# Performance work log

Measured on AMD Instinct MI355X. Metric: run time of the kernel, lower is better.

## Reference

```python
import jax, jax.numpy as jnp
import numpy as np

ALPHA = 0.9
T = 809          # doc_len_limit hard-coded in fofe_tricontext_encoder
M = 16           # opt['max_len'] (cand_len_limit)
BN_EPS = 1e-5


def _cand_indices(T, M):
    # Enumeration order matches get_sample_index: outer over start s, inner over span.
    s_list, e_list = [], []
    for s in range(T):
        for span in range(min(M, T - s)):
            s_list.append(s)
            e_list.append(s + span)
    return np.asarray(s_list, np.int32), np.asarray(e_list, np.int32)

_S_IDX, _E_IDX = _cand_indices(T, M)          # [N_CANDS] = [12824]
_SPAN = (_E_IDX - _S_IDX).astype(np.int64)
# FOFE decay coefficient alpha^(e-s+1) for subtracting the prefix before the span
_COEF = (ALPHA ** (_SPAN + 1)).astype(np.float32)
# Lower-triangular FOFE prefix operator: A[t,k] = alpha^(t-k) for k<=t
_DIFF = np.subtract.outer(np.arange(T), np.arange(T))
_AFWD = np.where(_DIFF >= 0, ALPHA ** np.maximum(_DIFF, 0), 0.0).astype(np.float32)


def _bn(x, g, b, m, v):
    return (x - m) * jax.lax.rsqrt(v + BN_EPS) * g + b


def _forward(doc_emb, query_emb, W1, g1, b1, m1, v1, W2, g2, b2, m2, v2, W3):
    B, Tt, Dd = doc_emb.shape
    A = jnp.asarray(_AFWD)
    # forward FOFE prefixes F[t] = sum_{k<=t} alpha^(t-k) x[k]; inverse FOFE suffixes
    F = jnp.einsum('tk,bkd->btd', A, doc_emb)          # [B,T,Dd]
    R = jnp.einsum('tk,bkd->btd', A.T, doc_emb)        # [B,T,Dd]
    Fp = jnp.concatenate([jnp.zeros((B, 1, Dd), F.dtype), F], axis=1)   # Fp[:,s]=F[s-1]
    Rp = jnp.concatenate([R, jnp.zeros((B, 1, Dd), R.dtype)], axis=1)   # Rp[:,e+1]
    s_idx = jnp.asarray(_S_IDX)
    e_idx = jnp.asarray(_E_IDX)
    coef = jnp.asarray(_COEF)
    lctx = Fp[:, s_idx]                                 # left context excl cand
    cand = F[:, e_idx] - coef[None, :, None] * Fp[:, s_idx]  # FOFE of span [s,e]
    rctx = Rp[:, e_idx + 1]                             # right context excl cand
    doc_fofe = jnp.concatenate([lctx, cand, rctx], axis=-1)  # [B,N,3*Dd]
    # query FOFE (fofe_linear): z = sum_t alpha^(Lq-1-t) q[t]
    Lq = query_emb.shape[1]
    w = (ALPHA ** jnp.arange(Lq - 1, -1, -1, dtype=jnp.float32))
    qf = jnp.einsum('t,btd->bd', w, query_emb)          # [B,E]
    N = doc_fofe.shape[1]
    qf_b = jnp.broadcast_to(qf[:, None, :], (B, N, qf.shape[-1]))
    dq = jnp.concatenate([doc_fofe, qf_b], axis=-1)     # [B,N,3*Dd+E]
    x = dq.reshape(B * N, -1)
    h = jax.nn.relu(_bn(x @ W1.T, g1, b1, m1, v1))      # 1x1 conv == GEMM
    h = jax.nn.relu(_bn(h @ W2.T, g2, b2, m2, v2))
    out = (h @ W3.T).reshape(B, N, 2)                   # 2 class scores per candidate
    return out


def setup_inputs() -> dict:
    key = jax.random.key(0)
    ks = jax.random.split(key, 13)
    B, Lq, Dd, E = 4, 30, 304, 300
    Cin, H4, H2 = 3 * Dd + E, 1024, 512
    return {
        'doc_emb': jax.random.normal(ks[0], (B, T, Dd), jnp.float32),
        'query_emb': jax.random.normal(ks[1], (B, Lq, E), jnp.float32),
        'W1': jax.random.normal(ks[2], (H4, Cin), jnp.float32) / np.sqrt(Cin),
        'g1': jax.random.normal(ks[3], (H4,), jnp.float32),
        'b1': jax.random.normal(ks[4], (H4,), jnp.float32),
        'm1': jax.random.normal(ks[5], (H4,), jnp.float32),
        'v1': jax.random.uniform(ks[6], (H4,), jnp.float32),
        'W2': jax.random.normal(ks[7], (H2, H4), jnp.float32) / np.sqrt(H4),
        'g2': jax.random.normal(ks[8], (H2,), jnp.float32),
        'b2': jax.random.normal(ks[9], (H2,), jnp.float32),
        'm2': jax.random.normal(ks[10], (H2,), jnp.float32),
        'v2': jax.random.uniform(ks[11], (H2,), jnp.float32),
        'W3': jax.random.normal(ks[12], (2, H2), jnp.float32) / np.sqrt(H2),
    }


def reference(doc_emb, query_emb, W1, g1, b1, m1, v1, W2, g2, b2, m2, v2, W3):
    return _forward(doc_emb, query_emb, W1, g1, b1, m1, v1, W2, g2, b2, m2, v2, W3)
```

## Files before the change

### kernel.cpp

```cpp
#include <hip/hip_runtime.h>
#include <hip/hip_fp16.h>
#include <string.h>

#define T_LEN   809
#define DD      304
#define EE      300
#define LQ      30
#define NCAND   12824
#define NPAD    12928
#define CIN     1212
#define H1      1024
#define H2      512
#define BATCH   4
#define MROWS_F (BATCH * NPAD)
#define KS      320
#define TPAD    3328
#define NROWS_U 3240

#define MP_W1      208
#define MP_W2      4048
#define MP_BIAS2   6096
#define MP_BASE    6098
#define MP_RMAP    7122
#define MP_TOTAL   7324

__device__ __constant__ float c_coef[16] = {
  0.9f, 0.81f, 0.729f, 0.6561f, 0.59049f, 0.531441f, 0.4782969f, 0.43046721f,
  0.387420489f, 0.3486784401f, 0.31381059609f, 0.282429536481f,
  0.2541865828329f, 0.22876792454961f, 0.205891132094649f, 0.1853020188851841f
};

__device__ __forceinline__ unsigned short f2h(float f) {
  const __half h = __float2half(f);
  return __half_as_ushort(h);
}
__device__ __forceinline__ unsigned int hadd2u(unsigned int a, unsigned int b) {
  const __half2 r = __hadd2(*reinterpret_cast<const __half2*>(&a),
                            *reinterpret_cast<const __half2*>(&b));
  return *reinterpret_cast<const unsigned int*>(&r);
}
__device__ __forceinline__ unsigned int comb2h(unsigned int ul, unsigned int uc,
                                               unsigned int ue, __half2 ncf2) {
  const __half2 t = __hfma2(*reinterpret_cast<const __half2*>(&uc), ncf2,
                            *reinterpret_cast<const __half2*>(&ue));
  const __half2 r = __hadd2(*reinterpret_cast<const __half2*>(&ul), t);
  unsigned int ru = *reinterpret_cast<const unsigned int*>(&r);
  ru &= ~(((ru >> 15) & 0x10001u) * 0xFFFFu);
  return ru;
}

typedef const __attribute__((address_space(1))) unsigned int GU32;
typedef __attribute__((address_space(3))) unsigned int LU32;
__device__ __forceinline__ void async16(const unsigned short* g, unsigned short* l) {
  __builtin_amdgcn_global_load_lds((GU32*)g, (LU32*)l, 16, 0, 0);
}

__global__ __launch_bounds__(256) void k_prep(const float* __restrict__ doc,
                                              const float* __restrict__ qe,
                                              const float* __restrict__ W1,
                                              const float* __restrict__ g1,
                                              const float* __restrict__ b1,
                                              const float* __restrict__ m1,
                                              const float* __restrict__ v1,
                                              const float* __restrict__ W2,
                                              const float* __restrict__ g2,
                                              const float* __restrict__ b2,
                                              const float* __restrict__ m2,
                                              const float* __restrict__ v2,
                                              unsigned short* __restrict__ Fz,
                                              unsigned short* __restrict__ Rz,
                                              unsigned short* __restrict__ Wlc,
                                              unsigned short* __restrict__ Wr,
                                              unsigned short* __restrict__ W2b,
                                              float* __restrict__ bias2,
                                              float* __restrict__ baseW,
                                              unsigned int* __restrict__ rowmap)
{
  __shared__ float qs[EE];
  const int vb  = blockIdx.x;
  const int tid = threadIdx.x;

  if (vb < MP_W1) {
    const int dchunk = vb & 1;
    const int rest   = vb >> 1;
    const int tchunk = rest % 13;
    const int b      = (rest / 13) & 3;
    const int dir    = rest / 52;
    const int d  = dchunk * 256 + tid;
    const int t0 = tchunk * 64;
    if (dir == 0) {
      if (tchunk == 0 && d < KS) Fz[((size_t)b * 810) * KS + d] = 0;
      if (d >= DD) return;
      const float* db = doc + (size_t)b * T_LEN * DD + d;
      int start = t0 - 96; if (start < 0) start = 0;
      int end = t0 + 63; if (end > T_LEN - 1) end = T_LEN - 1;
      float s = 0.f;
      int t = start;
      #pragma unroll 4
      for (; t < t0; ++t) s = fmaf(0.9f, s, db[(size_t)t * DD]);
      #pragma unroll 4
      for (; t <= end; ++t) {
        s = fmaf(0.9f, s, db[(size_t)t * DD]);
        Fz[((size_t)b * 810 + 1 + t) * KS + d] = f2h(s);
      }
    } else {
      if (tchunk == 0 && d < KS) Rz[((size_t)b * 810 + 809) * KS + d] = 0;
      if (d >= DD) return;
      const float* db = doc + (size_t)b * T_LEN * DD + d;
      int t1 = t0 + 63; if (t1 > T_LEN - 1) t1 = T_LEN - 1;
      int start = t1 + 96; if (start > T_LEN - 1) start = T_LEN - 1;
      float s = 0.f;
      int t = start;
      #pragma unroll 4
      for (; t > t1; --t) s = fmaf(0.9f, s, db[(size_t)t * DD]);
      #pragma unroll 4
      for (; t >= t0; --t) {
        s = fmaf(0.9f, s, db[(size_t)t * DD]);
        Rz[((size_t)b * 810 + t) * KS + d] = f2h(s);
      }
    }
  } else if (vb < MP_W2) {
    const int e = (vb - MP_W1) * 256 + tid;
    const int j = e / KS;
    const int k = e - j * KS;
    int jj, koff; unsigned short* dst; size_t idx;
    if (j < 1024)      { jj = j;        koff = k;       dst = Wlc; idx = (size_t)j * KS + k; }
    else if (j < 2048) { jj = j - 1024; koff = 304 + k; dst = Wlc; idx = (size_t)j * KS + k; }
    else               { jj = j - 2048; koff = 608 + k; dst = Wr;  idx = (size_t)(j - 2048) * KS + k; }
    float w = 0.f;
    if (k < 304) w = W1[(size_t)jj * CIN + koff] * g1[jj] * rsqrtf(v1[jj] + 1e-5f);
    dst[idx] = f2h(w);
  } else if (vb < MP_BIAS2) {
    const int e = (vb - MP_W2) * 256 + tid;
    const int j = e >> 10;
    const int k = e & 1023;
    const float w = W2[(size_t)j * H1 + k] * g2[j] * rsqrtf(v2[j] + 1e-5f);
    W2b[(size_t)j * H1 + k] = f2h(w);
  } else if (vb < MP_BASE) {
    const int i = (vb - MP_BIAS2) * 256 + tid;
    if (i < H2) {
      const float s = g2[i] * rsqrtf(v2[i] + 1e-5f);
      bias2[i] = b2[i] - m2[i] * s;
    }
  } else if (vb < MP_RMAP) {
    const int flat = vb - MP_BASE;
    const int b  = flat >> 8;
    const int jg = flat & 255;
    const float* q = qe + (size_t)b * LQ * EE;
    for (int k = tid; k < EE; k += 256) {
      float s = 0.f;
      for (int t = 0; t < LQ; ++t) s = fmaf(s, 0.9f, q[(size_t)t * EE + k]);
      qs[k] = s;
    }
    __syncthreads();
    const int wv   = tid >> 6;
    const int lane = tid & 63;
    const int j = jg * 4 + wv;
    const float* w = W1 + (size_t)j * CIN + 912;
    float acc = 0.f;
    for (int k = lane; k < EE; k += 64) acc = fmaf(qs[k], w[k], acc);
    #pragma unroll
    for (int off = 32; off; off >>= 1) acc += __shfl_down(acc, off);
    if (lane == 0) {
      const float sc = g1[j] * rsqrtf(v1[j] + 1e-5f);
      baseW[(size_t)b * 2048 + j]        = b1[j] - m1[j] * sc + acc * sc;
      baseW[(size_t)b * 2048 + 1024 + j] = 0.f;
    }
  } else {
    const int g = (vb - MP_RMAP) * 256 + tid;
    const int b  = g / NPAD;
    const int rr = g - b * NPAD;
    unsigned int mv = 0;
    if (rr < NCAND) {
      int s, span;
      if (rr < 12704) { s = rr >> 4; span = rr & 15; }
      else {
        const int x = rr - 12704;
        int d = 0;
        while (d < 14 && x >= (15 * (d + 1) - ((d + 1) * d) / 2)) ++d;
        span = x - (15 * d - (d * (d - 1)) / 2);
        s = 794 + d;
      }
      const unsigned int srow = (unsigned int)(b * 810 + s);
      const unsigned int erow = (unsigned int)(b * 810 + s + span + 1);
      mv = srow | (erow << 12) | ((unsigned int)span << 24);
    }
    rowmap[g] = mv;
  }
}

typedef __attribute__((ext_vector_type(8))) short frag8;
typedef __attribute__((ext_vector_type(4))) float f32x4;

#define GEMM_KLOOP(A_, B_, K_)                                                   \
  __shared__ __align__(16) unsigned short As[2 * 128 * 32];                      \
  __shared__ __align__(16) unsigned short Bs[2 * 128 * 32];                      \
  const int tid  = threadIdx.x;                                                  \
  const int lane = tid & 63;                                                     \
  const int wv   = tid >> 6;                                                     \
  const int wm   = wv & 1, wn = wv >> 1;                                         \
  const int lr = lane >> 2;                                                      \
  const int lc = lane & 3;                                                       \
  const int sc = lc ^ ((lr >> 1) & 3);                                           \
  const unsigned short* gA = A_ + ((size_t)bm * 128 + wv * 32 + lr) * K_ + sc * 8; \
  const unsigned short* gB = B_ + ((size_t)bn * 128 + wv * 32 + lr) * K_ + sc * 8; \
  const size_t row16 = (size_t)16 * K_;                                          \
  f32x4 acc[4][4];                                                               \
  _Pragma("unroll")                                                              \
  for (int i = 0; i < 4; ++i)                                                    \
    _Pragma("unroll")                                                            \
    for (int j = 0; j < 4; ++j) acc[i][j] = (f32x4){0.f, 0.f, 0.f, 0.f};         \
  const int arow = lane & 15;                                                    \
  const int pg   = (lane >> 4) ^ ((arow >> 1) & 3);                              \
  const int aoff = (wm * 64 + arow) * 32 + pg * 8;                               \
  const int boff = (wn * 64 + arow) * 32 + pg * 8;                               \
  async16(gA,         &As[wv * 1024]);                                           \
  async16(gA + row16, &As[wv * 1024 + 512]);                                     \
  async16(gB,         &Bs[wv * 1024]);                                           \
  async16(gB + row16, &Bs[wv * 1024 + 512]);                                     \
  asm volatile("s_waitcnt vmcnt(0)" ::: "memory");                               \
  __builtin_amdgcn_sched_barrier(0);                                             \
  for (int kc = 0; kc < K_; kc += 32) {                                          \
    const int cb = (kc >> 5) & 1, nb = cb ^ 1;                                   \
    __builtin_amdgcn_s_barrier();                                                \
    __builtin_amdgcn_sched_barrier(0);                                           \
    if (kc + 32 < K_) {                                                          \
      async16(gA + kc + 32,         &As[nb * 4096 + wv * 1024]);                 \
      async16(gA + kc + 32 + row16, &As[nb * 4096 + wv * 1024 + 512]);           \
      async16(gB + kc + 32,         &Bs[nb * 4096 + wv * 1024]);                 \
      async16(gB + kc + 32 + row16, &Bs[nb * 4096 + wv * 1024 + 512]);           \
    }                                                                            \
    __builtin_amdgcn_sched_barrier(0);                                           \
    frag8 a[4], b[4];                                                            \
    _Pragma("unroll")                                                            \
    for (int i = 0; i < 4; ++i) a[i] = *(const frag8*)&As[cb * 4096 + aoff + i * 512]; \
    _Pragma("unroll")                                                            \
    for (int i = 0; i < 4; ++i) b[i] = *(const frag8*)&Bs[cb * 4096 + boff + i * 512]; \
    __builtin_amdgcn_s_setprio(1);                                               \
    _Pragma("unroll")                                                            \
    for (int i = 0; i < 4; ++i)                                                  \
      _Pragma("unroll")                                                          \
      for (int j = 0; j < 4; ++j)                                                \
        acc[i][j] = __builtin_amdgcn_mfma_f32_16x16x32_f16(a[i], b[j], acc[i][j], 0, 0, 0); \
    __builtin_amdgcn_s_setprio(0);                                               \
    __builtin_amdgcn_sched_barrier(0);                                           \
    if (kc + 32 < K_) { asm volatile("s_waitcnt vmcnt(0)" ::: "memory"); }       \
    __builtin_amdgcn_sched_barrier(0);                                           \
  }

__global__ __launch_bounds__(256, 4) void k_ugemm(const unsigned short* __restrict__ Fz,
                                                  const unsigned short* __restrict__ Wlc,
                                                  const unsigned short* __restrict__ Rz,
                                                  const unsigned short* __restrict__ Wr,
                                                  const float* __restrict__ baseW,
                                                  unsigned short* __restrict__ UF,
                                                  unsigned short* __restrict__ UR)
{
  int bx = blockIdx.x;
  const int isUF = (bx < 416);
  const unsigned short *Ap, *Bp; unsigned short* Cp; int bn, bm, Nout;
  if (isUF) { Ap = Fz; Bp = Wlc; Cp = UF; bn = bx & 15; bm = bx >> 4; Nout = 2048; }
  else { bx -= 416; Ap = Rz; Bp = Wr; Cp = UR; bn = bx & 7; bm = bx >> 3; Nout = 1024; }
  GEMM_KLOOP(Ap, Bp, KS)

  __syncthreads();
  unsigned short* scr = &As[wv * 1152];
  const int grp   = lane >> 4;
  const int ccolb = bn * 128 + wn * 64;
  const int rowl  = lane >> 2;
  const int cg    = (lane & 3) * 16;
  #pragma unroll
  for (int i = 0; i < 4; ++i) {
    #pragma unroll
    for (int j = 0; j < 4; ++j)
      #pragma unroll
      for (int r = 0; r < 4; ++r) {
        const int col = ccolb + j * 16 + arow;
        float v = acc[i][j][r];
        if (isUF) {
          const int row = bm * 128 + wm * 64 + grp * 4 + i * 16 + r;
          int bb = row / 810; if (bb > 3) bb = 3;
          v += baseW[(size_t)bb * 2048 + col];
        }
        scr[(grp * 4 + r) * 72 + j * 16 + arow] = f2h(v);
      }
    asm volatile("s_waitcnt lgkmcnt(0)" ::: "memory");
    __builtin_amdgcn_sched_barrier(0);
    const uint4 w0 = *(const uint4*)&scr[rowl * 72 + cg];
    const uint4 w1 = *(const uint4*)&scr[rowl * 72 + cg + 8];
    const size_t grow = (size_t)(bm * 128 + wm * 64 + i * 16 + rowl) * Nout + ccolb + cg;
    *(uint4*)&Cp[grow]     = w0;
    *(uint4*)&Cp[grow + 8] = w1;
    __builtin_amdgcn_sched_barrier(0);
  }
}

__global__ __launch_bounds__(256) void k_ucr(const unsigned short* __restrict__ UF,
                                             const unsigned short* __restrict__ UR,
                                             unsigned short* __restrict__ UCR)
{
  const int c = blockIdx.x * 256 + threadIdx.x;
  if (c >= NROWS_U * 128) return;
  const int t  = c >> 7;
  const int kk = (c & 127) * 8;
  const uint4 a = *(const uint4*)(UF + (size_t)t * 2048 + 1024 + kk);
  const uint4 b = *(const uint4*)(UR + (size_t)t * 1024 + kk);
  uint4 o;
  o.x = hadd2u(a.x, b.x);
  o.y = hadd2u(a.y, b.y);
  o.z = hadd2u(a.z, b.z);
  o.w = hadd2u(a.w, b.w);
  *(uint4*)(UCR + (size_t)t * 1024 + kk) = o;
}

__global__ __launch_bounds__(512, 4) void k_gemm2f(const unsigned short* __restrict__ UF,
                                                   const unsigned short* __restrict__ UCR,
                                                   const unsigned short* __restrict__ W2b,
                                                   const unsigned int* __restrict__ rowmap,
                                                   const float* __restrict__ bias,
                                                   const float* __restrict__ W3,
                                                   float* __restrict__ out)
{
  __shared__ __align__(16) unsigned short As2[2 * 128 * 32];
  __shared__ __align__(16) unsigned short Bs2[2 * 256 * 32];

  const int orig = blockIdx.x;
  const int wg = (orig & 7) * 101 + (orig >> 3);
  const int bm = wg >> 1, bn = wg & 1;

  const int tid  = threadIdx.x;
  const int lane = tid & 63;
  const int w    = tid >> 6;
  const int wm   = w & 1;
  const int wn   = w >> 1;
  const int arow = lane & 15;
  const int lr   = lane >> 2;
  const int lc   = lane & 3;
  const int sc   = lc ^ ((lr >> 1) & 3);

  const int rA    = tid >> 2;
  const int cA    = tid & 3;
  const int physA = cA ^ ((rA >> 1) & 3);
  const unsigned int mv = rowmap[bm * 128 + rA];
  const __half2 ncf2 = __float2half2_rn(-c_coef[mv >> 24]);
  const unsigned short* pUL = UF  + (size_t)(mv & 4095) * 2048 + cA * 8;
  const unsigned short* pUE = UCR + (size_t)((mv >> 12) & 4095) * 1024 + cA * 8;

  const unsigned short* gB = W2b + ((size_t)(bn * 256 + w * 32 + lr)) * H1 + sc * 8;

  const int pg   = (lane >> 4) ^ ((arow >> 1) & 3);
  const int aoff = (wm * 64 + arow) * 32 + pg * 8;
  const int boff = (wn * 64 + arow) * 32 + pg * 8;

  f32x4 acc[4][4];
  #pragma unroll
  for (int i = 0; i < 4; ++i)
    #pragma unroll
    for (int j = 0; j < 4; ++j) acc[i][j] = (f32x4){0.f, 0.f, 0.f, 0.f};

  uint4 vulN = *(const uint4*)(pUL);
  uint4 vucN = *(const uint4*)(pUL + 1024);
  uint4 vueN = *(const uint4*)(pUE);
  {
    unsigned short* lB = &Bs2[w * 1024];
    async16(gB,           lB);
    async16(gB + 16 * H1, lB + 512);
  }
  {
    uint4 o;
    o.x = comb2h(vulN.x, vucN.x, vueN.x, ncf2);
    o.y = comb2h(vulN.y, vucN.y, vueN.y, ncf2);
    o.z = comb2h(vulN.z, vucN.z, vueN.z, ncf2);
    o.w = comb2h(vulN.w, vucN.w, vueN.w, ncf2);
    *(uint4*)&As2[rA * 32 + physA * 8] = o;
  }
  vulN = *(const uint4*)(pUL + 32);
  vucN = *(const uint4*)(pUL + 1024 + 32);
  vueN = *(const uint4*)(pUE + 32);
  asm volatile("s_waitcnt vmcnt(3) lgkmcnt(0)" ::: "memory");
  __builtin_amdgcn_sched_barrier(0);

  for (int k = 0; k < 32; ++k) {
    const int cur = k & 1, nxt = cur ^ 1;
    __builtin_amdgcn_s_barrier();
    __builtin_amdgcn_sched_barrier(0);
    if (k < 31) {
      const int kn = (k + 1) * 32;
      unsigned short* lB = &Bs2[nxt * 8192 + w * 1024];
      async16(gB + kn,           lB);
      async16(gB + kn + 16 * H1, lB + 512);
      __builtin_amdgcn_sched_barrier(0);
      asm volatile("s_waitcnt vmcnt(2)" ::: "memory");
      __builtin_amdgcn_sched_barrier(0);
      uint4 o;
      o.x = comb2h(vulN.x, vucN.x, vueN.x, ncf2);
      o.y = comb2h(vulN.y, vucN.y, vueN.y, ncf2);
      o.z = comb2h(vulN.z, vucN.z, vueN.z, ncf2);
      o.w = comb2h(vulN.w, vucN.w, vueN.w, ncf2);
      *(uint4*)&As2[nxt * 4096 + rA * 32 + physA * 8] = o;
      if (k < 30) {
        const int kg = (k + 2) * 32;
        vulN = *(const uint4*)(pUL + kg);
        vucN = *(const uint4*)(pUL + 1024 + kg);
        vueN = *(const uint4*)(pUE + kg);
      }
    }
    __builtin_amdgcn_sched_barrier(0);
    frag8 a[4], b[4];
    #pragma unroll
    for (int i = 0; i < 4; ++i) a[i] = *(const frag8*)&As2[cur * 4096 + aoff + i * 512];
    #pragma unroll
    for (int j = 0; j < 4; ++j) b[j] = *(const frag8*)&Bs2[cur * 8192 + boff + j * 512];
    __builtin_amdgcn_s_setprio(1);
    #pragma unroll
    for (int i = 0; i < 4; ++i)
      #pragma unroll
      for (int j = 0; j < 4; ++j)
        acc[i][j] = __builtin_amdgcn_mfma_f32_16x16x32_f16(a[i], b[j], acc[i][j], 0, 0, 0);
    __builtin_amdgcn_s_setprio(0);
    __builtin_amdgcn_sched_barrier(0);
    if (k < 30)       { asm volatile("s_waitcnt vmcnt(3)" ::: "memory"); }
    else if (k == 30) { asm volatile("s_waitcnt vmcnt(0)" ::: "memory"); }
    __builtin_amdgcn_sched_barrier(0);
  }

  __syncthreads();
  float* redf = (float*)As2;

  float bj[4], w0v[4], w1v[4];
  #pragma unroll
  for (int j = 0; j < 4; ++j) {
    const int col = bn * 256 + wn * 64 + j * 16 + arow;
    bj[j]  = bias[col];
    w0v[j] = W3[col];
    w1v[j] = W3[H2 + col];
  }
  const int grp = lane >> 4;
  #pragma unroll
  for (int i = 0; i < 4; ++i)
    #pragma unroll
    for (int r = 0; r < 4; ++r) {
      float q0 = 0.f, q1 = 0.f;
      #pragma unroll
      for (int j = 0; j < 4; ++j) {
        float v = acc[i][j][r] + bj[j];
        v = v > 0.f ? v : 0.f;
        q0 = fmaf(v, w0v[j], q0);
        q1 = fmaf(v, w1v[j], q1);
      }
      #pragma unroll
      for (int m = 1; m < 16; m <<= 1) { q0 += __shfl_xor(q0, m); q1 += __shfl_xor(q1, m); }
      if (arow == 0) {
        const int rl = wm * 64 + i * 16 + grp * 4 + r;
        redf[(rl * 4 + wn) * 2]     = q0;
        redf[(rl * 4 + wn) * 2 + 1] = q1;
      }
    }
  __syncthreads();
  if (tid < 256) {
    const int rl = tid >> 1, s = tid & 1;
    const float v = redf[(rl * 4 + 0) * 2 + s] + redf[(rl * 4 + 1) * 2 + s]
                  + redf[(rl * 4 + 2) * 2 + s] + redf[(rl * 4 + 3) * 2 + s];
    const int row = bm * 128 + rl;
    const int b   = row / NPAD;
    const int rr  = row - b * NPAD;
    if (rr < NCAND) atomicAdd(out + ((size_t)b * NCAND + rr) * 2 + s, v);
  }
}

extern "C" void kernel_launch(void* const* d_in, const int* in_sizes, int n_in,
                              void* d_out, int out_size, void* d_ws, size_t ws_size,
                              hipStream_t stream)
{
  const float* doc = (const float*)d_in[0];
  const float* qe  = (const float*)d_in[1];
  const float* W1  = (const float*)d_in[2];
  const float* g1  = (const float*)d_in[3];
  const float* b1  = (const float*)d_in[4];
  const float* m1  = (const float*)d_in[5];
  const float* v1  = (const float*)d_in[6];
  const float* W2  = (const float*)d_in[7];
  const float* g2  = (const float*)d_in[8];
  const float* b2  = (const float*)d_in[9];
  const float* m2  = (const float*)d_in[10];
  const float* v2  = (const float*)d_in[11];
  const float* W3  = (const float*)d_in[12];
  float* out = (float*)d_out;

  char* ws = (char*)d_ws;
  size_t off = 0;
  auto alloc = [&](size_t bytes) -> void* {
    void* p = ws + off;
    off = (off + bytes + 255) & ~(size_t)255;
    return p;
  };
  unsigned short* Fz    = (unsigned short*)alloc((size_t)TPAD * KS * 2);
  unsigned short* Rz    = (unsigned short*)alloc((size_t)TPAD * KS * 2);
  unsigned short* Wlc   = (unsigned short*)alloc((size_t)2048 * KS * 2);
  unsigned short* Wr    = (unsigned short*)alloc((size_t)1024 * KS * 2);
  unsigned short* W2b   = (unsigned short*)alloc((size_t)H2 * H1 * 2);
  float*          bias2 = (float*)alloc((size_t)H2 * 4);
  float*          baseW = (float*)alloc((size_t)BATCH * 2048 * 4);
  unsigned short* UF    = (unsigned short*)alloc((size_t)TPAD * 2048 * 2);
  unsigned short* UR    = (unsigned short*)alloc((size_t)TPAD * 1024 * 2);
  unsigned short* UCR   = (unsigned short*)alloc((size_t)NROWS_U * 1024 * 2);
  unsigned int*   rowmap= (unsigned int*)alloc((size_t)MROWS_F * 4);
  (void)ws_size;

  k_prep<<<dim3(MP_TOTAL), 256, 0, stream>>>(doc, qe, W1, g1, b1, m1, v1,
                                             W2, g2, b2, m2, v2,
                                             Fz, Rz, Wlc, Wr, W2b, bias2, baseW, rowmap);
  k_ugemm<<<dim3(416 + 208), 256, 0, stream>>>(Fz, Wlc, Rz, Wr, baseW, UF, UR);
  k_ucr<<<dim3((NROWS_U * 128 + 255) / 256), 256, 0, stream>>>(UF, UR, UCR);
  k_gemm2f<<<dim3(808), 512, 0, stream>>>(UF, UCR, W2b, rowmap, bias2, W3, out);
}
```

Baseline: 195.7 us.

## Fuse UR GEMM and UCR add into paired UF-upper GEMM blocks

The separate k_ucr elementwise kernel and the UR intermediate buffer are removed. Blocks that compute the upper half of UF now also compute the R-projection GEMM, interleaving K-steps of both into two accumulator sets. In the epilogue they write both UF's upper half and UCR = F+R directly. This saves a kernel launch and the UR write/read round trip. The cost is a doubled accumulator count in the paired blocks, which raises register pressure, and uneven work between the two block types.

Result: no change. 197.1 us (+0.7%).

```diff
diff --git a/kernel.cpp b/kernel.cpp
--- a/kernel.cpp
+++ b/kernel.cpp
@@ -33,11 +33,6 @@
 __device__ __forceinline__ unsigned short f2h(float f) {
   const __half h = __float2half(f);
   return __half_as_ushort(h);
-}
-__device__ __forceinline__ unsigned int hadd2u(unsigned int a, unsigned int b) {
-  const __half2 r = __hadd2(*reinterpret_cast<const __half2*>(&a),
-                            *reinterpret_cast<const __half2*>(&b));
-  return *reinterpret_cast<const unsigned int*>(&r);
 }
 __device__ __forceinline__ unsigned int comb2h(unsigned int ul, unsigned int uc,
                                                unsigned int ue, __half2 ncf2) {
@@ -192,125 +187,194 @@
 typedef __attribute__((ext_vector_type(8))) short frag8;
 typedef __attribute__((ext_vector_type(4))) float f32x4;
 
-#define GEMM_KLOOP(A_, B_, K_)                                                   \
-  __shared__ __align__(16) unsigned short As[2 * 128 * 32];                      \
-  __shared__ __align__(16) unsigned short Bs[2 * 128 * 32];                      \
-  const int tid  = threadIdx.x;                                                  \
-  const int lane = tid & 63;                                                     \
-  const int wv   = tid >> 6;                                                     \
-  const int wm   = wv & 1, wn = wv >> 1;                                         \
-  const int lr = lane >> 2;                                                      \
-  const int lc = lane & 3;                                                       \
-  const int sc = lc ^ ((lr >> 1) & 3);                                           \
-  const unsigned short* gA = A_ + ((size_t)bm * 128 + wv * 32 + lr) * K_ + sc * 8; \
-  const unsigned short* gB = B_ + ((size_t)bn * 128 + wv * 32 + lr) * K_ + sc * 8; \
-  const size_t row16 = (size_t)16 * K_;                                          \
-  f32x4 acc[4][4];                                                               \
-  _Pragma("unroll")                                                              \
-  for (int i = 0; i < 4; ++i)                                                    \
-    _Pragma("unroll")                                                            \
-    for (int j = 0; j < 4; ++j) acc[i][j] = (f32x4){0.f, 0.f, 0.f, 0.f};         \
-  const int arow = lane & 15;                                                    \
-  const int pg   = (lane >> 4) ^ ((arow >> 1) & 3);                              \
-  const int aoff = (wm * 64 + arow) * 32 + pg * 8;                               \
-  const int boff = (wn * 64 + arow) * 32 + pg * 8;                               \
-  async16(gA,         &As[wv * 1024]);                                           \
-  async16(gA + row16, &As[wv * 1024 + 512]);                                     \
-  async16(gB,         &Bs[wv * 1024]);                                           \
-  async16(gB + row16, &Bs[wv * 1024 + 512]);                                     \
-  asm volatile("s_waitcnt vmcnt(0)" ::: "memory");                               \
-  __builtin_amdgcn_sched_barrier(0);                                             \
-  for (int kc = 0; kc < K_; kc += 32) {                                          \
-    const int cb = (kc >> 5) & 1, nb = cb ^ 1;                                   \
-    __builtin_amdgcn_s_barrier();                                                \
-    __builtin_amdgcn_sched_barrier(0);                                           \
-    if (kc + 32 < K_) {                                                          \
-      async16(gA + kc + 32,         &As[nb * 4096 + wv * 1024]);                 \
-      async16(gA + kc + 32 + row16, &As[nb * 4096 + wv * 1024 + 512]);           \
-      async16(gB + kc + 32,         &Bs[nb * 4096 + wv * 1024]);                 \
-      async16(gB + kc + 32 + row16, &Bs[nb * 4096 + wv * 1024 + 512]);           \
-    }                                                                            \
-    __builtin_amdgcn_sched_barrier(0);                                           \
-    frag8 a[4], b[4];                                                            \
-    _Pragma("unroll")                                                            \
-    for (int i = 0; i < 4; ++i) a[i] = *(const frag8*)&As[cb * 4096 + aoff + i * 512]; \
-    _Pragma("unroll")                                                            \
-    for (int i = 0; i < 4; ++i) b[i] = *(const frag8*)&Bs[cb * 4096 + boff + i * 512]; \
-    __builtin_amdgcn_s_setprio(1);                                               \
-    _Pragma("unroll")                                                            \
-    for (int i = 0; i < 4; ++i)                                                  \
-      _Pragma("unroll")                                                          \
-      for (int j = 0; j < 4; ++j)                                                \
-        acc[i][j] = __builtin_amdgcn_mfma_f32_16x16x32_f16(a[i], b[j], acc[i][j], 0, 0, 0); \
-    __builtin_amdgcn_s_setprio(0);                                               \
-    __builtin_amdgcn_sched_barrier(0);                                           \
-    if (kc + 32 < K_) { asm volatile("s_waitcnt vmcnt(0)" ::: "memory"); }       \
-    __builtin_amdgcn_sched_barrier(0);                                           \
-  }
-
-__global__ __launch_bounds__(256, 4) void k_ugemm(const unsigned short* __restrict__ Fz,
-                                                  const unsigned short* __restrict__ Wlc,
-                                                  const unsigned short* __restrict__ Rz,
-                                                  const unsigned short* __restrict__ Wr,
-                                                  const float* __restrict__ baseW,
-                                                  unsigned short* __restrict__ UF,
-                                                  unsigned short* __restrict__ UR)
+__global__ __launch_bounds__(256) void k_ugemm(const unsigned short* __restrict__ Fz,
+                                               const unsigned short* __restrict__ Wlc,
+                                               const unsigned short* __restrict__ Rz,
+                                               const unsigned short* __restrict__ Wr,
+                                               const float* __restrict__ baseW,
+                                               unsigned short* __restrict__ UF,
+                                               unsigned short* __restrict__ UCR)
 {
+  __shared__ __align__(16) unsigned short As[2 * 128 * 32];
+  __shared__ __align__(16) unsigned short Bs[2 * 128 * 32];
+  const int tid  = threadIdx.x;
+  const int lane = tid & 63;
+  const int wv   = tid >> 6;
+  const int wm   = wv & 1, wn = wv >> 1;
+  const int lr = lane >> 2;
+  const int lc = lane & 3;
+  const int sc = lc ^ ((lr >> 1) & 3);
+  const int arow = lane & 15;
+  const int pg   = (lane >> 4) ^ ((arow >> 1) & 3);
+  const int aoff = (wm * 64 + arow) * 32 + pg * 8;
+  const int boff = (wn * 64 + arow) * 32 + pg * 8;
+  const size_t row16 = (size_t)16 * KS;
+  const int grp = lane >> 4, rowl = lane >> 2, cg = (lane & 3) * 16;
+  unsigned short* scr = &As[wv * 1152];
+
   int bx = blockIdx.x;
-  const int isUF = (bx < 416);
-  const unsigned short *Ap, *Bp; unsigned short* Cp; int bn, bm, Nout;
-  if (isUF) { Ap = Fz; Bp = Wlc; Cp = UF; bn = bx & 15; bm = bx >> 4; Nout = 2048; }
-  else { bx -= 416; Ap = Rz; Bp = Wr; Cp = UR; bn = bx & 7; bm = bx >> 3; Nout = 1024; }
-  GEMM_KLOOP(Ap, Bp, KS)
-
-  __syncthreads();
-  unsigned short* scr = &As[wv * 1152];
-  const int grp   = lane >> 4;
-  const int ccolb = bn * 128 + wn * 64;
-  const int rowl  = lane >> 2;
-  const int cg    = (lane & 3) * 16;
-  #pragma unroll
-  for (int i = 0; i < 4; ++i) {
-    #pragma unroll
-    for (int j = 0; j < 4; ++j)
-      #pragma unroll
-      for (int r = 0; r < 4; ++r) {
-        const int col = ccolb + j * 16 + arow;
-        float v = acc[i][j][r];
-        if (isUF) {
+  const int paired = bx >= 208;
+  if (paired) bx -= 208;
+  const int bm = bx >> 3, bn = bx & 7;
+  const size_t aro = ((size_t)bm * 128 + wv * 32 + lr) * KS + sc * 8;
+
+  if (!paired) {
+    const unsigned short* gA = Fz  + aro;
+    const unsigned short* gB = Wlc + ((size_t)(bn * 128) + wv * 32 + lr) * KS + sc * 8;
+    f32x4 acc[4][4];
+    #pragma unroll
+    for (int i = 0; i < 4; ++i)
+      #pragma unroll
+      for (int j = 0; j < 4; ++j) acc[i][j] = (f32x4){0.f, 0.f, 0.f, 0.f};
+    async16(gA,         &As[wv * 1024]);
+    async16(gA + row16, &As[wv * 1024 + 512]);
+    async16(gB,         &Bs[wv * 1024]);
+    async16(gB + row16, &Bs[wv * 1024 + 512]);
+    asm volatile("s_waitcnt vmcnt(0)" ::: "memory");
+    __builtin_amdgcn_sched_barrier(0);
+    for (int kc = 0; kc < KS; kc += 32) {
+      const int cb = (kc >> 5) & 1, nb = cb ^ 1;
+      __builtin_amdgcn_s_barrier();
+      __builtin_amdgcn_sched_barrier(0);
+      if (kc + 32 < KS) {
+        async16(gA + kc + 32,         &As[nb * 4096 + wv * 1024]);
+        async16(gA + kc + 32 + row16, &As[nb * 4096 + wv * 1024 + 512]);
+        async16(gB + kc + 32,         &Bs[nb * 4096 + wv * 1024]);
+        async16(gB + kc + 32 + row16, &Bs[nb * 4096 + wv * 1024 + 512]);
+      }
+      __builtin_amdgcn_sched_barrier(0);
+      frag8 a[4], b[4];
+      #pragma unroll
+      for (int i = 0; i < 4; ++i) a[i] = *(const frag8*)&As[cb * 4096 + aoff + i * 512];
+      #pragma unroll
+      for (int i = 0; i < 4; ++i) b[i] = *(const frag8*)&Bs[cb * 4096 + boff + i * 512];
+      __builtin_amdgcn_s_setprio(1);
+      #pragma unroll
+      for (int i = 0; i < 4; ++i)
+        #pragma unroll
+        for (int j = 0; j < 4; ++j)
+          acc[i][j] = __builtin_amdgcn_mfma_f32_16x16x32_f16(a[i], b[j], acc[i][j], 0, 0, 0);
+      __builtin_amdgcn_s_setprio(0);
+      __builtin_amdgcn_sched_barrier(0);
+      if (kc + 32 < KS) { asm volatile("s_waitcnt vmcnt(0)" ::: "memory"); }
+      __builtin_amdgcn_sched_barrier(0);
+    }
+    __syncthreads();
+    const int ccolb = bn * 128 + wn * 64;
+    #pragma unroll
+    for (int i = 0; i < 4; ++i) {
+      #pragma unroll
+      for (int j = 0; j < 4; ++j)
+        #pragma unroll
+        for (int r = 0; r < 4; ++r) {
+          const int col = ccolb + j * 16 + arow;
           const int row = bm * 128 + wm * 64 + grp * 4 + i * 16 + r;
           int bb = row / 810; if (bb > 3) bb = 3;
-          v += baseW[(size_t)bb * 2048 + col];
+          scr[(grp * 4 + r) * 72 + j * 16 + arow] = f2h(acc[i][j][r] + baseW[(size_t)bb * 2048 + col]);
         }
-        scr[(grp * 4 + r) * 72 + j * 16 + arow] = f2h(v);
-      }
-    asm volatile("s_waitcnt lgkmcnt(0)" ::: "memory");
+      asm volatile("s_waitcnt lgkmcnt(0)" ::: "memory");
+      __builtin_amdgcn_sched_barrier(0);
+      const uint4 w0 = *(const uint4*)&scr[rowl * 72 + cg];
+      const uint4 w1 = *(const uint4*)&scr[rowl * 72 + cg + 8];
+      const size_t grow = (size_t)(bm * 128 + wm * 64 + i * 16 + rowl) * 2048 + ccolb + cg;
+      *(uint4*)&UF[grow]     = w0;
+      *(uint4*)&UF[grow + 8] = w1;
+      __builtin_amdgcn_sched_barrier(0);
+    }
+  } else {
+    const unsigned short* gAF = Fz  + aro;
+    const unsigned short* gAR = Rz  + aro;
+    const unsigned short* gBL = Wlc + ((size_t)(1024 + bn * 128) + wv * 32 + lr) * KS + sc * 8;
+    const unsigned short* gBR = Wr  + ((size_t)(bn * 128) + wv * 32 + lr) * KS + sc * 8;
+    f32x4 accF[4][4], accR[4][4];
+    #pragma unroll
+    for (int i = 0; i < 4; ++i)
+      #pragma unroll
+      for (int j = 0; j < 4; ++j) {
+        accF[i][j] = (f32x4){0.f, 0.f, 0.f, 0.f};
+        accR[i][j] = (f32x4){0.f, 0.f, 0.f, 0.f};
+      }
+    async16(gAF,         &As[wv * 1024]);
+    async16(gAF + row16, &As[wv * 1024 + 512]);
+    async16(gBL,         &Bs[wv * 1024]);
+    async16(gBL + row16, &Bs[wv * 1024 + 512]);
+    asm volatile("s_waitcnt vmcnt(0)" ::: "memory");
     __builtin_amdgcn_sched_barrier(0);
-    const uint4 w0 = *(const uint4*)&scr[rowl * 72 + cg];
-    const uint4 w1 = *(const uint4*)&scr[rowl * 72 + cg + 8];
-    const size_t grow = (size_t)(bm * 128 + wm * 64 + i * 16 + rowl) * Nout + ccolb + cg;
-    *(uint4*)&Cp[grow]     = w0;
-    *(uint4*)&Cp[grow + 8] = w1;
-    __builtin_amdgcn_sched_barrier(0);
-  }
-}
-
-__global__ __launch_bounds__(256) void k_ucr(const unsigned short* __restrict__ UF,
-                                             const unsigned short* __restrict__ UR,
-                                             unsigned short* __restrict__ UCR)
-{
-  const int c = blockIdx.x * 256 + threadIdx.x;
-  if (c >= NROWS_U * 128) return;
-  const int t  = c >> 7;
-  const int kk = (c & 127) * 8;
-  const uint4 a = *(const uint4*)(UF + (size_t)t * 2048 + 1024 + kk);
-  const uint4 b = *(const uint4*)(UR + (size_t)t * 1024 + kk);
-  uint4 o;
-  o.x = hadd2u(a.x, b.x);
-  o.y = hadd2u(a.y, b.y);
-  o.z = hadd2u(a.z, b.z);
-  o.w = hadd2u(a.w, b.w);
-  *(uint4*)(UCR + (size_t)t * 1024 + kk) = o;
+    #pragma unroll 2
+    for (int s = 0; s < 20; ++s) {
+      const int cb = s & 1, nb = cb ^ 1;
+      __builtin_amdgcn_s_barrier();
+      __builtin_amdgcn_sched_barrier(0);
+      if (s < 19) {
+        const int kn = ((s + 1) >> 1) * 32;
+        const unsigned short* a_ = ((s + 1) & 1) ? gAR : gAF;
+        const unsigned short* b_ = ((s + 1) & 1) ? gBR : gBL;
+        async16(a_ + kn,         &As[nb * 4096 + wv * 1024]);
+        async16(a_ + kn + row16, &As[nb * 4096 + wv * 1024 + 512]);
+        async16(b_ + kn,         &Bs[nb * 4096 + wv * 1024]);
+        async16(b_ + kn + row16, &Bs[nb * 4096 + wv * 1024 + 512]);
+      }
+      __builtin_amdgcn_sched_barrier(0);
+      frag8 a[4], b[4];
+      #pragma unroll
+      for (int i = 0; i < 4; ++i) a[i] = *(const frag8*)&As[cb * 4096 + aoff + i * 512];
+      #pragma unroll
+      for (int i = 0; i < 4; ++i) b[i] = *(const frag8*)&Bs[cb * 4096 + boff + i * 512];
+      __builtin_amdgcn_s_setprio(1);
+      if (s & 1) {
+        #pragma unroll
+        for (int i = 0; i < 4; ++i)
+          #pragma unroll
+          for (int j = 0; j < 4; ++j)
+            accR[i][j] = __builtin_amdgcn_mfma_f32_16x16x32_f16(a[i], b[j], accR[i][j], 0, 0, 0);
+      } else {
+        #pragma unroll
+        for (int i = 0; i < 4; ++i)
+          #pragma unroll
+          for (int j = 0; j < 4; ++j)
+            accF[i][j] = __builtin_amdgcn_mfma_f32_16x16x32_f16(a[i], b[j], accF[i][j], 0, 0, 0);
+      }
+      __builtin_amdgcn_s_setprio(0);
+      __builtin_amdgcn_sched_barrier(0);
+      if (s < 19) { asm volatile("s_waitcnt vmcnt(0)" ::: "memory"); }
+      __builtin_amdgcn_sched_barrier(0);
+    }
+    __syncthreads();
+    const int ccolb = bn * 128 + wn * 64;
+    #pragma unroll
+    for (int i = 0; i < 4; ++i) {
+      #pragma unroll
+      for (int j = 0; j < 4; ++j)
+        #pragma unroll
+        for (int r = 0; r < 4; ++r)
+          scr[(grp * 4 + r) * 72 + j * 16 + arow] = f2h(accF[i][j][r]);
+      asm volatile("s_waitcnt lgkmcnt(0)" ::: "memory");
+      __builtin_amdgcn_sched_barrier(0);
+      {
+        const uint4 w0 = *(const uint4*)&scr[rowl * 72 + cg];
+        const uint4 w1 = *(const uint4*)&scr[rowl * 72 + cg + 8];
+        const size_t grow = (size_t)(bm * 128 + wm * 64 + i * 16 + rowl) * 2048 + 1024 + ccolb + cg;
+        *(uint4*)&UF[grow]     = w0;
+        *(uint4*)&UF[grow + 8] = w1;
+      }
+      __builtin_amdgcn_sched_barrier(0);
+      #pragma unroll
+      for (int j = 0; j < 4; ++j)
+        #pragma unroll
+        for (int r = 0; r < 4; ++r)
+          scr[(grp * 4 + r) * 72 + j * 16 + arow] = f2h(accF[i][j][r] + accR[i][j][r]);
+      asm volatile("s_waitcnt lgkmcnt(0)" ::: "memory");
+      __builtin_amdgcn_sched_barrier(0);
+      {
+        const uint4 w0 = *(const uint4*)&scr[rowl * 72 + cg];
+        const uint4 w1 = *(const uint4*)&scr[rowl * 72 + cg + 8];
+        const size_t grow = (size_t)(bm * 128 + wm * 64 + i * 16 + rowl) * 1024 + ccolb + cg;
+        *(uint4*)&UCR[grow]     = w0;
+        *(uint4*)&UCR[grow + 8] = w1;
+      }
+      __builtin_amdgcn_sched_barrier(0);
+    }
+  }
 }
 
 __global__ __launch_bounds__(512, 4) void k_gemm2f(const unsigned short* __restrict__ UF,
@@ -502,15 +566,13 @@
   float*          bias2 = (float*)alloc((size_t)H2 * 4);
   float*          baseW = (float*)alloc((size_t)BATCH * 2048 * 4);
   unsigned short* UF    = (unsigned short*)alloc((size_t)TPAD * 2048 * 2);
-  unsigned short* UR    = (unsigned short*)alloc((size_t)TPAD * 1024 * 2);
-  unsigned short* UCR   = (unsigned short*)alloc((size_t)NROWS_U * 1024 * 2);
+  unsigned short* UCR   = (unsigned short*)alloc((size_t)TPAD * 1024 * 2);
   unsigned int*   rowmap= (unsigned int*)alloc((size_t)MROWS_F * 4);
   (void)ws_size;
 
   k_prep<<<dim3(MP_TOTAL), 256, 0, stream>>>(doc, qe, W1, g1, b1, m1, v1,
                                              W2, g2, b2, m2, v2,
                                              Fz, Rz, Wlc, Wr, W2b, bias2, baseW, rowmap);
-  k_ugemm<<<dim3(416 + 208), 256, 0, stream>>>(Fz, Wlc, Rz, Wr, baseW, UF, UR);
-  k_ucr<<<dim3((NROWS_U * 128 + 255) / 256), 256, 0, stream>>>(UF, UR, UCR);
+  k_ugemm<<<dim3(416), 256, 0, stream>>>(Fz, Wlc, Rz, Wr, baseW, UF, UCR);
   k_gemm2f<<<dim3(808), 512, 0, stream>>>(UF, UCR, W2b, rowmap, bias2, W3, out);
 }
```
